# Kernel optimization log

Hardware: AMD Instinct MI355X
Metric: run time of the kernel (lower is better)

## Reference

```python
import jax, jax.numpy as jnp
import numpy as np

D = 128      # embedding dim
T = 8        # message passing rounds (config.training.T)
NV = 4000    # n_vars
NL = 2 * NV  # n_literals
NC = 16000   # n_clauses


def setup_inputs() -> dict:
    key = jax.random.key(0)
    ks = jax.random.split(key, 12)
    s = np.float32(1.0 / np.sqrt(D))
    return {
        "L_state": jax.random.normal(ks[0], (1, NL, D), jnp.float32),
        "C_state": jax.random.normal(ks[1], (1, NC, D), jnp.float32),
        "hidden_L": jnp.zeros((1, NL, D), jnp.float32),
        "hidden_C": jnp.zeros((1, NC, D), jnp.float32),
        # 0/1 literal-clause incidence, ~40 clauses per literal
        "M": (jax.random.uniform(ks[2], (NL, NC)) < 0.0025).astype(jnp.float32),
        "n_vars": NV,
        "W_lc": jax.random.normal(ks[3], (D, D), jnp.float32) * s,
        "b_lc": jnp.zeros((D,), jnp.float32),
        "W_cl": jax.random.normal(ks[4], (D, D), jnp.float32) * s,
        "b_cl": jnp.zeros((D,), jnp.float32),
        "Wih_C": jax.random.normal(ks[5], (4 * D, D), jnp.float32) * s,
        "Whh_C": jax.random.normal(ks[6], (4 * D, D), jnp.float32) * s,
        "bih_C": jnp.zeros((4 * D,), jnp.float32),
        "bhh_C": jnp.zeros((4 * D,), jnp.float32),
        "Wih_L": jax.random.normal(ks[7], (4 * D, 2 * D), jnp.float32) * s,
        "Whh_L": jax.random.normal(ks[8], (4 * D, D), jnp.float32) * s,
        "bih_L": jnp.zeros((4 * D,), jnp.float32),
        "bhh_L": jnp.zeros((4 * D,), jnp.float32),
    }


def lstm_cell(x, h, c, Wih, Whh, bih, bhh):
    # torch nn.LSTM gate order: i, f, g, o
    gates = x @ Wih.T + bih + h @ Whh.T + bhh
    i, f, g, o = jnp.split(gates, 4, axis=-1)
    c_new = jax.nn.sigmoid(f) * c + jax.nn.sigmoid(i) * jnp.tanh(g)
    h_new = jax.nn.sigmoid(o) * jnp.tanh(c_new)
    return h_new, c_new


def reference(L_state, C_state, hidden_L, hidden_C, M, n_vars,
              W_lc, b_lc, W_cl, b_cl,
              Wih_C, Whh_C, bih_C, bhh_C,
              Wih_L, Whh_L, bih_L, bhh_L):
    # Replicates torch flip() as written: slices dim 0 (size 1), so this is
    # effectively identity for n_vars >= 1 (first slice is empty, second is x).
    def flip(x):
        return jnp.concatenate([x[n_vars:2 * n_vars], x[0:n_vars]], axis=0)

    def step(carry, _):
        L, hL, hC = carry
        LC_pre = L @ W_lc.T + b_lc                        # (1, NL, D)
        LC_msgs = jnp.einsum('lc,sld->scd', M, LC_pre)    # M^T @ pre: (1, NC, D)
        Cs, hC = lstm_cell(LC_msgs, hC, hC, Wih_C, Whh_C, bih_C, bhh_C)
        CL_pre = Cs @ W_cl.T + b_cl                       # (1, NC, D)
        CL_msgs = jnp.einsum('lc,scd->sld', M, CL_pre)    # M @ pre: (1, NL, D)
        inp = jnp.concatenate([CL_msgs, flip(L)], axis=2) # (1, NL, 2D)
        L, hL = lstm_cell(inp, hL, hL, Wih_L, Whh_L, bih_L, bhh_L)
        return (L, hL, hC), None

    (L_final, _, _), _ = jax.lax.scan(step, (L_state, hidden_L, hidden_C), None, length=T)
    return L_final
```

## Files before the change

### kernel.cpp

```cpp
#include <hip/hip_runtime.h>

#define DD   128
#define NL   8000
#define NC   16000
#define TSTEPS 8
#define ROWW 96
#define COLW 64
#define OS   33
#define SPLITS8 (32 * OS)
#define SPLIT   (SPLITS8 * 8)

typedef __attribute__((ext_vector_type(8))) short short8;
typedef __attribute__((ext_vector_type(4))) float f32x4;

__device__ __forceinline__ float frcp(float x) { return __builtin_amdgcn_rcpf(x); }
__device__ __forceinline__ float sigm(float x) { return frcp(1.f + __expf(-x)); }
__device__ __forceinline__ float tanh_(float x) {
  float e = __expf(2.f * x);
  return 1.f - 2.f * frcp(e + 1.f);
}
__device__ __forceinline__ void add4(float4& a, const float4 b) {
  a.x += b.x; a.y += b.y; a.z += b.z; a.w += b.w;
}
__device__ __forceinline__ unsigned short bfround(float v) {
  unsigned u = __float_as_uint(v);
  return (unsigned short)((u + 0x7FFF + ((u >> 16) & 1)) >> 16);
}
__device__ __forceinline__ float bf2f(unsigned short b) {
  return __uint_as_float(((unsigned)b) << 16);
}
__device__ __forceinline__ int4 packi4(const unsigned short* p) {
  return make_int4(p[0] | ((int)p[1] << 16), p[2] | ((int)p[3] << 16),
                   p[4] | ((int)p[5] << 16), p[6] | ((int)p[7] << 16));
}

__device__ __forceinline__ void store_oct3(unsigned short* A, int oct, int m,
                                           float4 a, float4 b) {
  float f[8] = {a.x, a.y, a.z, a.w, b.x, b.y, b.z, b.w};
  unsigned short h[8], md[8], lo[8];
  #pragma unroll
  for (int j = 0; j < 8; ++j) {
    h[j] = bfround(f[j]);
    float r1 = f[j] - bf2f(h[j]);
    md[j] = bfround(r1);
    float r2 = r1 - bf2f(md[j]);
    lo[j] = bfround(r2);
  }
  int base = (oct * OS + m) * 8;
  *(int4*)(A + base)             = packi4(h);
  *(int4*)(A + SPLIT + base)     = packi4(md);
  *(int4*)(A + 2 * SPLIT + base) = packi4(lo);
}


__global__ __launch_bounds__(256) void copy_f4(float4* __restrict__ dst, const float4* __restrict__ src, int n4) {
  int stride = gridDim.x * blockDim.x;
  for (int i = blockIdx.x * blockDim.x + threadIdx.x; i < n4; i += stride) dst[i] = src[i];
}

__global__ __launch_bounds__(256) void scan_M(const float4* __restrict__ M4,
                                              int* __restrict__ csr, int* __restrict__ csc,
                                              int* __restrict__ rcnt, int* __restrict__ ccnt) {
  const int total = (NL * NC) / 4;
  int stride = gridDim.x * blockDim.x;
  for (int i = blockIdx.x * blockDim.x + threadIdx.x; i < total; i += stride) {
    float4 v = M4[i];
    if (v.x == 0.f && v.y == 0.f && v.z == 0.f && v.w == 0.f) continue;
    int base = i * 4;
    int l = base / NC;
    int c0 = base - l * NC;
    float vv[4] = {v.x, v.y, v.z, v.w};
    #pragma unroll
    for (int e = 0; e < 4; ++e) {
      if (vv[e] != 0.f) {
        int c = c0 + e;
        int rp = atomicAdd(&rcnt[l], 1);
        if (rp < ROWW) csr[l * ROWW + rp] = c;
        int cp = atomicAdd(&ccnt[c], 1);
        if (cp < COLW) csc[c * COLW + cp] = l;
      }
    }
  }
}

__device__ __forceinline__ void split_store(float w, int idx, unsigned short* hi,
                                            unsigned short* md, unsigned short* lo) {
  unsigned short h = bfround(w);
  float r1 = w - bf2f(h);
  unsigned short m = bfround(r1);
  float r2 = r1 - bf2f(m);
  hi[idx] = h; md[idx] = m; lo[idx] = bfround(r2);
}

__global__ __launch_bounds__(256) void build_packC(
    const float* __restrict__ WihC, const float* __restrict__ Wlc, const float* __restrict__ WhhC,
    unsigned short* __restrict__ pkhi, unsigned short* __restrict__ pkmd, unsigned short* __restrict__ pklo) {
  int i = blockIdx.x * 256 + threadIdx.x;
  int k = i >> 9, n = i & 511;
  float w;
  if (k < 128) {
    float s = 0.f;
    for (int d = 0; d < 128; ++d) s += WihC[n * 128 + d] * Wlc[d * 128 + k];
    w = s;
  } else {
    w = WhhC[n * 128 + (k - 128)];
  }
  split_store(w, ((k >> 3) * 512 + n) * 8 + (k & 7), pkhi, pkmd, pklo);
}

__global__ __launch_bounds__(256) void build_packL(
    const float* __restrict__ WihL, const float* __restrict__ Wcl, const float* __restrict__ WhhL,
    unsigned short* __restrict__ pkhi, unsigned short* __restrict__ pkmd, unsigned short* __restrict__ pklo) {
  int i = blockIdx.x * 256 + threadIdx.x;
  int k = i >> 9, n = i & 511;
  float w;
  if (k < 128) {
    float s = 0.f;
    for (int d = 0; d < 128; ++d) s += WihL[n * 256 + d] * Wcl[d * 128 + k];
    w = s;
  } else if (k < 256) {
    w = WihL[n * 256 + k];
  } else {
    w = WhhL[n * 128 + (k - 256)];
  }
  split_store(w, ((k >> 3) * 512 + n) * 8 + (k & 7), pkhi, pkmd, pklo);
}

__global__ __launch_bounds__(256) void build_bias(
    const float* __restrict__ bihC, const float* __restrict__ bhhC,
    const float* __restrict__ WihC, const float* __restrict__ blc,
    const float* __restrict__ bihL, const float* __restrict__ bhhL,
    const float* __restrict__ WihL, const float* __restrict__ bcl,
    float* __restrict__ bsumC, float* __restrict__ bvecC,
    float* __restrict__ bsumL, float* __restrict__ bvecL) {
  int i = blockIdx.x * 256 + threadIdx.x;
  if (i < 512) {
    bsumC[i] = bihC[i] + bhhC[i];
    float s = 0.f;
    for (int d = 0; d < 128; ++d) s += WihC[i * 128 + d] * blc[d];
    bvecC[i] = s;
  } else if (i < 1024) {
    int n = i - 512;
    bsumL[n] = bihL[n] + bhhL[n];
    float s = 0.f;
    for (int d = 0; d < 128; ++d) s += WihL[n * 256 + d] * bcl[d];
    bvecL[n] = s;
  }
}

#define MFMA6(ACC, AH, AM, AL, BH, BM, BL)                                   \
  ACC = __builtin_amdgcn_mfma_f32_16x16x32_bf16(AH, BH, ACC, 0, 0, 0);       \
  ACC = __builtin_amdgcn_mfma_f32_16x16x32_bf16(AH, BM, ACC, 0, 0, 0);       \
  ACC = __builtin_amdgcn_mfma_f32_16x16x32_bf16(AM, BH, ACC, 0, 0, 0);       \
  ACC = __builtin_amdgcn_mfma_f32_16x16x32_bf16(AH, BL, ACC, 0, 0, 0);       \
  ACC = __builtin_amdgcn_mfma_f32_16x16x32_bf16(AL, BH, ACC, 0, 0, 0);       \
  ACC = __builtin_amdgcn_mfma_f32_16x16x32_bf16(AM, BM, ACC, 0, 0, 0);


__global__ __launch_bounds__(512, 2) void clause_mfma(
    const float* __restrict__ Lbuf, const int* __restrict__ csc, const int* __restrict__ ccnt,
    const unsigned short* __restrict__ pkhi, const unsigned short* __restrict__ pkmd,
    const unsigned short* __restrict__ pklo,
    const float* __restrict__ bsum, const float* __restrict__ bvec,
    float* __restrict__ hC, float* __restrict__ Cs) {
  __shared__ unsigned short A[3 * SPLIT];
  const int t = threadIdx.x;
  const int rowBase = blockIdx.x * 32;

  {
    const int r = t >> 4, sub = t & 15;
    const int c = rowBase + r;
    int cnt = ccnt[c]; int cl = cnt > COLW ? COLW : cnt;
    const int* lst = csc + c * COLW;
    float4 a0 = make_float4(0, 0, 0, 0), a1 = a0;
    for (int j = 0; j < cl; ++j) {
      const float4* s4 = (const float4*)(Lbuf + (size_t)lst[j] * DD + sub * 8);
      add4(a0, s4[0]); add4(a1, s4[1]);
    }
    store_oct3(A, sub, r, a0, a1);
    const float4* h4 = (const float4*)(hC + (size_t)c * DD + sub * 8);
    store_oct3(A, 16 + sub, r, h4[0], h4[1]);
  }
  __syncthreads();

  const int w = t >> 6, l = t & 63;
  const int quad = l >> 4, lane16 = l & 15;
  const int cw = w * 16 + lane16;
  f32x4 acc[2][4];
  #pragma unroll
  for (int mt = 0; mt < 2; ++mt)
    #pragma unroll
    for (int g = 0; g < 4; ++g) acc[mt][g] = (f32x4){0.f, 0.f, 0.f, 0.f};

  const short8* As = (const short8*)A;
  const short8* Bh = (const short8*)pkhi;
  const short8* Bm = (const short8*)pkmd;
  const short8* Bl = (const short8*)pklo;

  #pragma unroll 2
  for (int s = 0; s < 8; ++s) {
    int ao = (s * 4 + quad) * OS + lane16;
    short8 a0h = As[ao],                a1h = As[ao + 16];
    short8 a0m = As[SPLITS8 + ao],      a1m = As[SPLITS8 + ao + 16];
    short8 a0l = As[2 * SPLITS8 + ao],  a1l = As[2 * SPLITS8 + ao + 16];
    int bo = (s * 4 + quad) * 512 + cw;
    #pragma unroll
    for (int g = 0; g < 4; ++g) {
      short8 bh = Bh[bo + g * 128];
      short8 bm = Bm[bo + g * 128];
      short8 bl = Bl[bo + g * 128];
      MFMA6(acc[0][g], a0h, a0m, a0l, bh, bm, bl);
      MFMA6(acc[1][g], a1h, a1m, a1l, bh, bm, bl);
    }
  }

  float bs_[4], bv_[4];
  #pragma unroll
  for (int g = 0; g < 4; ++g) { bs_[g] = bsum[g * 128 + cw]; bv_[g] = bvec[g * 128 + cw]; }
  #pragma unroll
  for (int mt = 0; mt < 2; ++mt) {
    #pragma unroll
    for (int reg = 0; reg < 4; ++reg) {
      int row = rowBase + mt * 16 + quad * 4 + reg;
      float deg = (float)ccnt[row];
      float co = hC[(size_t)row * DD + cw];
      float iv = acc[mt][0][reg] + bs_[0] + deg * bv_[0];
      float fv = acc[mt][1][reg] + bs_[1] + deg * bv_[1];
      float gv = acc[mt][2][reg] + bs_[2] + deg * bv_[2];
      float ov = acc[mt][3][reg] + bs_[3] + deg * bv_[3];
      float cn = sigm(fv) * co + sigm(iv) * tanh_(gv);
      hC[(size_t)row * DD + cw] = cn;
      Cs[(size_t)row * DD + cw] = sigm(ov) * tanh_(cn);
    }
  }
}

__global__ __launch_bounds__(512, 2) void literal_mfma(
    const float* __restrict__ Cs, const int* __restrict__ csr, const int* __restrict__ rcnt,
    const unsigned short* __restrict__ pkhi, const unsigned short* __restrict__ pkmd,
    const unsigned short* __restrict__ pklo,
    const float* __restrict__ bsum, const float* __restrict__ bvec,
    float* __restrict__ hL, float* __restrict__ Lbuf) {
  __shared__ unsigned short A[3 * SPLIT];
  const int t = threadIdx.x;
  const int rowBase = blockIdx.x * 32;
  const int r = t >> 4, sub = t & 15;
  const int lr = rowBase + r;

  {
    int cnt = rcnt[lr]; int cl = cnt > ROWW ? ROWW : cnt;
    const int* lst = csr + lr * ROWW;
    float4 a0 = make_float4(0, 0, 0, 0), a1 = a0;
    for (int j = 0; j < cl; ++j) {
      const float4* s4 = (const float4*)(Cs + (size_t)lst[j] * DD + sub * 8);
      add4(a0, s4[0]); add4(a1, s4[1]);
    }
    store_oct3(A, sub, r, a0, a1);
    const float4* l4 = (const float4*)(Lbuf + (size_t)lr * DD + sub * 8);
    store_oct3(A, 16 + sub, r, l4[0], l4[1]);
  }
  __syncthreads();

  const int w = t >> 6, l = t & 63;
  const int quad = l >> 4, lane16 = l & 15;
  const int cw = w * 16 + lane16;
  f32x4 acc[2][4];
  #pragma unroll
  for (int mt = 0; mt < 2; ++mt)
    #pragma unroll
    for (int g = 0; g < 4; ++g) acc[mt][g] = (f32x4){0.f, 0.f, 0.f, 0.f};

  const short8* As = (const short8*)A;
  const short8* Bh = (const short8*)pkhi;
  const short8* Bm = (const short8*)pkmd;
  const short8* Bl = (const short8*)pklo;

  #pragma unroll 2
  for (int s = 0; s < 8; ++s) {
    int ao = (s * 4 + quad) * OS + lane16;
    short8 a0h = As[ao],                a1h = As[ao + 16];
    short8 a0m = As[SPLITS8 + ao],      a1m = As[SPLITS8 + ao + 16];
    short8 a0l = As[2 * SPLITS8 + ao],  a1l = As[2 * SPLITS8 + ao + 16];
    int bo = (s * 4 + quad) * 512 + cw;
    #pragma unroll
    for (int g = 0; g < 4; ++g) {
      short8 bh = Bh[bo + g * 128];
      short8 bm = Bm[bo + g * 128];
      short8 bl = Bl[bo + g * 128];
      MFMA6(acc[0][g], a0h, a0m, a0l, bh, bm, bl);
      MFMA6(acc[1][g], a1h, a1m, a1l, bh, bm, bl);
    }
  }

  __syncthreads();
  {
    const float4* h4 = (const float4*)(hL + (size_t)lr * DD + sub * 8);
    store_oct3(A, sub, r, h4[0], h4[1]);
  }
  __syncthreads();

  #pragma unroll 2
  for (int s = 8; s < 12; ++s) {
    int ao = ((s - 8) * 4 + quad) * OS + lane16;
    short8 a0h = As[ao],                a1h = As[ao + 16];
    short8 a0m = As[SPLITS8 + ao],      a1m = As[SPLITS8 + ao + 16];
    short8 a0l = As[2 * SPLITS8 + ao],  a1l = As[2 * SPLITS8 + ao + 16];
    int bo = (s * 4 + quad) * 512 + cw;
    #pragma unroll
    for (int g = 0; g < 4; ++g) {
      short8 bh = Bh[bo + g * 128];
      short8 bm = Bm[bo + g * 128];
      short8 bl = Bl[bo + g * 128];
      MFMA6(acc[0][g], a0h, a0m, a0l, bh, bm, bl);
      MFMA6(acc[1][g], a1h, a1m, a1l, bh, bm, bl);
    }
  }

  float bs_[4], bv_[4];
  #pragma unroll
  for (int g = 0; g < 4; ++g) { bs_[g] = bsum[g * 128 + cw]; bv_[g] = bvec[g * 128 + cw]; }
  #pragma unroll
  for (int mt = 0; mt < 2; ++mt) {
    #pragma unroll
    for (int reg = 0; reg < 4; ++reg) {
      int row = rowBase + mt * 16 + quad * 4 + reg;
      float deg = (float)rcnt[row];
      float co = hL[(size_t)row * DD + cw];
      float iv = acc[mt][0][reg] + bs_[0] + deg * bv_[0];
      float fv = acc[mt][1][reg] + bs_[1] + deg * bv_[1];
      float gv = acc[mt][2][reg] + bs_[2] + deg * bv_[2];
      float ov = acc[mt][3][reg] + bs_[3] + deg * bv_[3];
      float cn = sigm(fv) * co + sigm(iv) * tanh_(gv);
      hL[(size_t)row * DD + cw] = cn;
      Lbuf[(size_t)row * DD + cw] = sigm(ov) * tanh_(cn);
    }
  }
}


extern "C" void kernel_launch(void* const* d_in, const int* in_sizes, int n_in,
                              void* d_out, int out_size, void* d_ws, size_t ws_size,
                              hipStream_t stream) {
  const float* L0   = (const float*)d_in[0];
  const float* hL0  = (const float*)d_in[2];
  const float* hC0  = (const float*)d_in[3];
  const float* M    = (const float*)d_in[4];
  const float* Wlc  = (const float*)d_in[6];
  const float* blc  = (const float*)d_in[7];
  const float* Wcl  = (const float*)d_in[8];
  const float* bcl  = (const float*)d_in[9];
  const float* WihC = (const float*)d_in[10];
  const float* WhhC = (const float*)d_in[11];
  const float* bihC = (const float*)d_in[12];
  const float* bhhC = (const float*)d_in[13];
  const float* WihL = (const float*)d_in[14];
  const float* WhhL = (const float*)d_in[15];
  const float* bihL = (const float*)d_in[16];
  const float* bhhL = (const float*)d_in[17];

  float* ws    = (float*)d_ws;
  float* hL    = ws;
  float* hC    = hL + NL * DD;
  float* Cs    = hC + NC * DD;
  float* bsumC = Cs + NC * DD;
  float* bvecC = bsumC + 512;
  float* bsumL = bvecC + 512;
  float* bvecL = bsumL + 512;
  unsigned short* pkChi = (unsigned short*)(bvecL + 512);
  unsigned short* pkCmd = pkChi + 256 * 512;
  unsigned short* pkClo = pkCmd + 256 * 512;
  unsigned short* pkLhi = pkClo + 256 * 512;
  unsigned short* pkLmd = pkLhi + 384 * 512;
  unsigned short* pkLlo = pkLmd + 384 * 512;
  int* csr  = (int*)(pkLlo + 384 * 512);
  int* csc  = csr + NL * ROWW;
  int* rcnt = csc + NC * COLW;
  int* ccnt = rcnt + NL;
  float* Lbuf = (float*)d_out;

  hipMemsetAsync(rcnt, 0, (NL + NC) * sizeof(int), stream);

  copy_f4<<<1024, 256, 0, stream>>>((float4*)Lbuf, (const float4*)L0,  NL * DD / 4);
  copy_f4<<<1024, 256, 0, stream>>>((float4*)hL,   (const float4*)hL0, NL * DD / 4);
  copy_f4<<<1024, 256, 0, stream>>>((float4*)hC,   (const float4*)hC0, NC * DD / 4);

  scan_M<<<4096, 256, 0, stream>>>((const float4*)M, csr, csc, rcnt, ccnt);

  build_packC<<<(256 * 512) / 256, 256, 0, stream>>>(WihC, Wlc, WhhC, pkChi, pkCmd, pkClo);
  build_packL<<<(384 * 512) / 256, 256, 0, stream>>>(WihL, Wcl, WhhL, pkLhi, pkLmd, pkLlo);
  build_bias<<<4, 256, 0, stream>>>(bihC, bhhC, WihC, blc, bihL, bhhL, WihL, bcl,
                                    bsumC, bvecC, bsumL, bvecL);

  for (int t = 0; t < TSTEPS; ++t) {
    clause_mfma<<<NC / 32, 512, 0, stream>>>(Lbuf, csc, ccnt, pkChi, pkCmd, pkClo,
                                             bsumC, bvecC, hC, Cs);
    literal_mfma<<<NL / 32, 512, 0, stream>>>(Cs, csr, rcnt, pkLhi, pkLmd, pkLlo,
                                              bsumL, bvecL, hL, Lbuf);
  }
}
```

Measured before the change: 1.473 ms.

## Fuse all message-passing steps into one persistent kernel with grid barriers

Replaces the 16 per-step clause/literal kernel launches and the three copy kernels with a single persistent kernel of 256 blocks. The blocks loop over tiles and use an atomic-counter grid barrier between phases. The literal phase now uses 16-row tiles with all three A segments held in shared memory at once, which avoids the mid-kernel reload and gives 500 tiles instead of 250. This removes launch gaps and tail effects between phases, but grid-stride tiling with 256 blocks gives uneven work per block (500 clause tiles), and the spin barrier relies on all blocks being co-resident.

```diff
diff --git a/kernel.cpp b/kernel.cpp
--- a/kernel.cpp
+++ b/kernel.cpp
@@ -6,9 +6,14 @@
 #define TSTEPS 8
 #define ROWW 96
 #define COLW 64
-#define OS   33
-#define SPLITS8 (32 * OS)
-#define SPLIT   (SPLITS8 * 8)
+#define NBLK 256
+#define CTILES (NC / 32)
+#define LTILES (NL / 16)
+
+#define CSTR 33
+#define CSPL (32 * CSTR * 8)
+#define LSTR 17
+#define LSPL (48 * LSTR * 8)
 
 typedef __attribute__((ext_vector_type(8))) short short8;
 typedef __attribute__((ext_vector_type(4))) float f32x4;
@@ -34,8 +39,8 @@
                    p[4] | ((int)p[5] << 16), p[6] | ((int)p[7] << 16));
 }
 
-__device__ __forceinline__ void store_oct3(unsigned short* A, int oct, int m,
-                                           float4 a, float4 b) {
+__device__ __forceinline__ void store_oct3C(unsigned short* A, int oct, int m,
+                                            float4 a, float4 b) {
   float f[8] = {a.x, a.y, a.z, a.w, b.x, b.y, b.z, b.w};
   unsigned short h[8], md[8], lo[8];
   #pragma unroll
@@ -46,17 +51,38 @@
     float r2 = r1 - bf2f(md[j]);
     lo[j] = bfround(r2);
   }
-  int base = (oct * OS + m) * 8;
-  *(int4*)(A + base)             = packi4(h);
-  *(int4*)(A + SPLIT + base)     = packi4(md);
-  *(int4*)(A + 2 * SPLIT + base) = packi4(lo);
-}
-
-
-__global__ __launch_bounds__(256) void copy_f4(float4* __restrict__ dst, const float4* __restrict__ src, int n4) {
-  int stride = gridDim.x * blockDim.x;
-  for (int i = blockIdx.x * blockDim.x + threadIdx.x; i < n4; i += stride) dst[i] = src[i];
-}
+  int base = (oct * CSTR + m) * 8;
+  *(int4*)(A + base)            = packi4(h);
+  *(int4*)(A + CSPL + base)     = packi4(md);
+  *(int4*)(A + 2 * CSPL + base) = packi4(lo);
+}
+
+__device__ __forceinline__ void store_half3L(unsigned short* A, int oct, int half, int m,
+                                             float4 a) {
+  float f[4] = {a.x, a.y, a.z, a.w};
+  unsigned short h[4], md[4], lo[4];
+  #pragma unroll
+  for (int j = 0; j < 4; ++j) {
+    h[j] = bfround(f[j]);
+    float r1 = f[j] - bf2f(h[j]);
+    md[j] = bfround(r1);
+    float r2 = r1 - bf2f(md[j]);
+    lo[j] = bfround(r2);
+  }
+  int base = (oct * LSTR + m) * 8 + half * 4;
+  *(int2*)(A + base)            = make_int2(h[0]  | ((int)h[1]  << 16), h[2]  | ((int)h[3]  << 16));
+  *(int2*)(A + LSPL + base)     = make_int2(md[0] | ((int)md[1] << 16), md[2] | ((int)md[3] << 16));
+  *(int2*)(A + 2 * LSPL + base) = make_int2(lo[0] | ((int)lo[1] << 16), lo[2] | ((int)lo[3] << 16));
+}
+
+#define MFMA6(ACC, AH, AM, AL, BH, BM, BL)                                   \
+  ACC = __builtin_amdgcn_mfma_f32_16x16x32_bf16(AH, BH, ACC, 0, 0, 0);       \
+  ACC = __builtin_amdgcn_mfma_f32_16x16x32_bf16(AH, BM, ACC, 0, 0, 0);       \
+  ACC = __builtin_amdgcn_mfma_f32_16x16x32_bf16(AM, BH, ACC, 0, 0, 0);       \
+  ACC = __builtin_amdgcn_mfma_f32_16x16x32_bf16(AH, BL, ACC, 0, 0, 0);       \
+  ACC = __builtin_amdgcn_mfma_f32_16x16x32_bf16(AL, BH, ACC, 0, 0, 0);       \
+  ACC = __builtin_amdgcn_mfma_f32_16x16x32_bf16(AM, BM, ACC, 0, 0, 0);
+
 
 __global__ __launch_bounds__(256) void scan_M(const float4* __restrict__ M4,
                                               int* __restrict__ csr, int* __restrict__ csc,
@@ -148,191 +174,181 @@
   }
 }
 
-#define MFMA6(ACC, AH, AM, AL, BH, BM, BL)                                   \
-  ACC = __builtin_amdgcn_mfma_f32_16x16x32_bf16(AH, BH, ACC, 0, 0, 0);       \
-  ACC = __builtin_amdgcn_mfma_f32_16x16x32_bf16(AH, BM, ACC, 0, 0, 0);       \
-  ACC = __builtin_amdgcn_mfma_f32_16x16x32_bf16(AM, BH, ACC, 0, 0, 0);       \
-  ACC = __builtin_amdgcn_mfma_f32_16x16x32_bf16(AH, BL, ACC, 0, 0, 0);       \
-  ACC = __builtin_amdgcn_mfma_f32_16x16x32_bf16(AL, BH, ACC, 0, 0, 0);       \
-  ACC = __builtin_amdgcn_mfma_f32_16x16x32_bf16(AM, BM, ACC, 0, 0, 0);
-
-
-__global__ __launch_bounds__(512, 2) void clause_mfma(
-    const float* __restrict__ Lbuf, const int* __restrict__ csc, const int* __restrict__ ccnt,
-    const unsigned short* __restrict__ pkhi, const unsigned short* __restrict__ pkmd,
-    const unsigned short* __restrict__ pklo,
-    const float* __restrict__ bsum, const float* __restrict__ bvec,
-    float* __restrict__ hC, float* __restrict__ Cs) {
-  __shared__ unsigned short A[3 * SPLIT];
+__device__ __forceinline__ void grid_barrier(int* cnt, int& gen) {
+  __syncthreads();
+  if (threadIdx.x == 0) {
+    __threadfence();
+    ++gen;
+    __hip_atomic_fetch_add(cnt, 1, __ATOMIC_ACQ_REL, __HIP_MEMORY_SCOPE_AGENT);
+    while (__hip_atomic_load(cnt, __ATOMIC_ACQUIRE, __HIP_MEMORY_SCOPE_AGENT) < gen * NBLK)
+      __builtin_amdgcn_s_sleep(1);
+    __threadfence();
+  }
+  __syncthreads();
+}
+
+
+__global__ __launch_bounds__(512, 4) void fused_steps(
+    const float* __restrict__ L0, const float* __restrict__ hL0, const float* __restrict__ hC0,
+    const int* __restrict__ csr, const int* __restrict__ csc,
+    const int* __restrict__ rcnt, const int* __restrict__ ccnt,
+    const unsigned short* __restrict__ pkChi, const unsigned short* __restrict__ pkCmd,
+    const unsigned short* __restrict__ pkClo,
+    const unsigned short* __restrict__ pkLhi, const unsigned short* __restrict__ pkLmd,
+    const unsigned short* __restrict__ pkLlo,
+    const float* __restrict__ bsumC, const float* __restrict__ bvecC,
+    const float* __restrict__ bsumL, const float* __restrict__ bvecL,
+    float* __restrict__ hL, float* __restrict__ hC, float* __restrict__ Cs,
+    float* __restrict__ Lbuf, int* __restrict__ bar) {
+  __shared__ unsigned short A[3 * CSPL];
+
   const int t = threadIdx.x;
-  const int rowBase = blockIdx.x * 32;
-
-  {
-    const int r = t >> 4, sub = t & 15;
-    const int c = rowBase + r;
-    int cnt = ccnt[c]; int cl = cnt > COLW ? COLW : cnt;
-    const int* lst = csc + c * COLW;
-    float4 a0 = make_float4(0, 0, 0, 0), a1 = a0;
-    for (int j = 0; j < cl; ++j) {
-      const float4* s4 = (const float4*)(Lbuf + (size_t)lst[j] * DD + sub * 8);
-      add4(a0, s4[0]); add4(a1, s4[1]);
-    }
-    store_oct3(A, sub, r, a0, a1);
-    const float4* h4 = (const float4*)(hC + (size_t)c * DD + sub * 8);
-    store_oct3(A, 16 + sub, r, h4[0], h4[1]);
-  }
-  __syncthreads();
-
+  const int b = blockIdx.x;
   const int w = t >> 6, l = t & 63;
   const int quad = l >> 4, lane16 = l & 15;
   const int cw = w * 16 + lane16;
-  f32x4 acc[2][4];
-  #pragma unroll
-  for (int mt = 0; mt < 2; ++mt)
-    #pragma unroll
-    for (int g = 0; g < 4; ++g) acc[mt][g] = (f32x4){0.f, 0.f, 0.f, 0.f};
-
-  const short8* As = (const short8*)A;
-  const short8* Bh = (const short8*)pkhi;
-  const short8* Bm = (const short8*)pkmd;
-  const short8* Bl = (const short8*)pklo;
-
-  #pragma unroll 2
-  for (int s = 0; s < 8; ++s) {
-    int ao = (s * 4 + quad) * OS + lane16;
-    short8 a0h = As[ao],                a1h = As[ao + 16];
-    short8 a0m = As[SPLITS8 + ao],      a1m = As[SPLITS8 + ao + 16];
-    short8 a0l = As[2 * SPLITS8 + ao],  a1l = As[2 * SPLITS8 + ao + 16];
-    int bo = (s * 4 + quad) * 512 + cw;
-    #pragma unroll
-    for (int g = 0; g < 4; ++g) {
-      short8 bh = Bh[bo + g * 128];
-      short8 bm = Bm[bo + g * 128];
-      short8 bl = Bl[bo + g * 128];
-      MFMA6(acc[0][g], a0h, a0m, a0l, bh, bm, bl);
-      MFMA6(acc[1][g], a1h, a1m, a1l, bh, bm, bl);
+  int gen = 0;
+
+  {
+    int gid = b * 512 + t, gstr = NBLK * 512;
+    for (int i = gid; i < NL * DD / 4; i += gstr) ((float4*)Lbuf)[i] = ((const float4*)L0)[i];
+    for (int i = gid; i < NL * DD / 4; i += gstr) ((float4*)hL)[i]   = ((const float4*)hL0)[i];
+    for (int i = gid; i < NC * DD / 4; i += gstr) ((float4*)hC)[i]   = ((const float4*)hC0)[i];
+  }
+
+  for (int step = 0; step < TSTEPS; ++step) {
+    grid_barrier(bar, gen);
+
+    for (int tile = b; tile < CTILES; tile += NBLK) {
+      const int rowBase = tile * 32;
+      {
+        const int r = t >> 4, sub = t & 15;
+        const int c = rowBase + r;
+        int cnt = ccnt[c]; int cl2 = cnt > COLW ? COLW : cnt;
+        const int* lst = csc + c * COLW;
+        float4 a0 = make_float4(0, 0, 0, 0), a1 = a0;
+        for (int j = 0; j < cl2; ++j) {
+          const float4* s4 = (const float4*)(Lbuf + (size_t)lst[j] * DD + sub * 8);
+          add4(a0, s4[0]); add4(a1, s4[1]);
+        }
+        store_oct3C(A, sub, r, a0, a1);
+        const float4* h4 = (const float4*)(hC + (size_t)c * DD + sub * 8);
+        store_oct3C(A, 16 + sub, r, h4[0], h4[1]);
+      }
+      __syncthreads();
+
+      f32x4 acc[2][4];
+      #pragma unroll
+      for (int mt = 0; mt < 2; ++mt)
+        #pragma unroll
+        for (int g = 0; g < 4; ++g) acc[mt][g] = (f32x4){0.f, 0.f, 0.f, 0.f};
+
+      const short8* As = (const short8*)A;
+      const short8* Bh = (const short8*)pkChi;
+      const short8* Bm = (const short8*)pkCmd;
+      const short8* Bl = (const short8*)pkClo;
+
+      #pragma unroll 2
+      for (int s = 0; s < 8; ++s) {
+        int ao = (s * 4 + quad) * CSTR + lane16;
+        short8 a0h = As[ao],                   a1h = As[ao + 16];
+        short8 a0m = As[CSPL / 8 + ao],        a1m = As[CSPL / 8 + ao + 16];
+        short8 a0l = As[2 * (CSPL / 8) + ao],  a1l = As[2 * (CSPL / 8) + ao + 16];
+        int bo = (s * 4 + quad) * 512 + cw;
+        #pragma unroll
+        for (int g = 0; g < 4; ++g) {
+          short8 bh = Bh[bo + g * 128];
+          short8 bm = Bm[bo + g * 128];
+          short8 bl = Bl[bo + g * 128];
+          MFMA6(acc[0][g], a0h, a0m, a0l, bh, bm, bl);
+          MFMA6(acc[1][g], a1h, a1m, a1l, bh, bm, bl);
+        }
+      }
+
+      float bs_[4], bv_[4];
+      #pragma unroll
+      for (int g = 0; g < 4; ++g) { bs_[g] = bsumC[g * 128 + cw]; bv_[g] = bvecC[g * 128 + cw]; }
+      #pragma unroll
+      for (int mt = 0; mt < 2; ++mt) {
+        #pragma unroll
+        for (int reg = 0; reg < 4; ++reg) {
+          int row = rowBase + mt * 16 + quad * 4 + reg;
+          float deg = (float)ccnt[row];
+          float co = hC[(size_t)row * DD + cw];
+          float iv = acc[mt][0][reg] + bs_[0] + deg * bv_[0];
+          float fv = acc[mt][1][reg] + bs_[1] + deg * bv_[1];
+          float gv = acc[mt][2][reg] + bs_[2] + deg * bv_[2];
+          float ov = acc[mt][3][reg] + bs_[3] + deg * bv_[3];
+          float cn = sigm(fv) * co + sigm(iv) * tanh_(gv);
+          hC[(size_t)row * DD + cw] = cn;
+          Cs[(size_t)row * DD + cw] = sigm(ov) * tanh_(cn);
+        }
+      }
+      __syncthreads();
     }
-  }
-
-  float bs_[4], bv_[4];
-  #pragma unroll
-  for (int g = 0; g < 4; ++g) { bs_[g] = bsum[g * 128 + cw]; bv_[g] = bvec[g * 128 + cw]; }
-  #pragma unroll
-  for (int mt = 0; mt < 2; ++mt) {
-    #pragma unroll
-    for (int reg = 0; reg < 4; ++reg) {
-      int row = rowBase + mt * 16 + quad * 4 + reg;
-      float deg = (float)ccnt[row];
-      float co = hC[(size_t)row * DD + cw];
-      float iv = acc[mt][0][reg] + bs_[0] + deg * bv_[0];
-      float fv = acc[mt][1][reg] + bs_[1] + deg * bv_[1];
-      float gv = acc[mt][2][reg] + bs_[2] + deg * bv_[2];
-      float ov = acc[mt][3][reg] + bs_[3] + deg * bv_[3];
-      float cn = sigm(fv) * co + sigm(iv) * tanh_(gv);
-      hC[(size_t)row * DD + cw] = cn;
-      Cs[(size_t)row * DD + cw] = sigm(ov) * tanh_(cn);
-    }
-  }
-}
-
-__global__ __launch_bounds__(512, 2) void literal_mfma(
-    const float* __restrict__ Cs, const int* __restrict__ csr, const int* __restrict__ rcnt,
-    const unsigned short* __restrict__ pkhi, const unsigned short* __restrict__ pkmd,
-    const unsigned short* __restrict__ pklo,
-    const float* __restrict__ bsum, const float* __restrict__ bvec,
-    float* __restrict__ hL, float* __restrict__ Lbuf) {
-  __shared__ unsigned short A[3 * SPLIT];
-  const int t = threadIdx.x;
-  const int rowBase = blockIdx.x * 32;
-  const int r = t >> 4, sub = t & 15;
-  const int lr = rowBase + r;
-
-  {
-    int cnt = rcnt[lr]; int cl = cnt > ROWW ? ROWW : cnt;
-    const int* lst = csr + lr * ROWW;
-    float4 a0 = make_float4(0, 0, 0, 0), a1 = a0;
-    for (int j = 0; j < cl; ++j) {
-      const float4* s4 = (const float4*)(Cs + (size_t)lst[j] * DD + sub * 8);
-      add4(a0, s4[0]); add4(a1, s4[1]);
-    }
-    store_oct3(A, sub, r, a0, a1);
-    const float4* l4 = (const float4*)(Lbuf + (size_t)lr * DD + sub * 8);
-    store_oct3(A, 16 + sub, r, l4[0], l4[1]);
-  }
-  __syncthreads();
-
-  const int w = t >> 6, l = t & 63;
-  const int quad = l >> 4, lane16 = l & 15;
-  const int cw = w * 16 + lane16;
-  f32x4 acc[2][4];
-  #pragma unroll
-  for (int mt = 0; mt < 2; ++mt)
-    #pragma unroll
-    for (int g = 0; g < 4; ++g) acc[mt][g] = (f32x4){0.f, 0.f, 0.f, 0.f};
-
-  const short8* As = (const short8*)A;
-  const short8* Bh = (const short8*)pkhi;
-  const short8* Bm = (const short8*)pkmd;
-  const short8* Bl = (const short8*)pklo;
-
-  #pragma unroll 2
-  for (int s = 0; s < 8; ++s) {
-    int ao = (s * 4 + quad) * OS + lane16;
-    short8 a0h = As[ao],                a1h = As[ao + 16];
-    short8 a0m = As[SPLITS8 + ao],      a1m = As[SPLITS8 + ao + 16];
-    short8 a0l = As[2 * SPLITS8 + ao],  a1l = As[2 * SPLITS8 + ao + 16];
-    int bo = (s * 4 + quad) * 512 + cw;
-    #pragma unroll
-    for (int g = 0; g < 4; ++g) {
-      short8 bh = Bh[bo + g * 128];
-      short8 bm = Bm[bo + g * 128];
-      short8 bl = Bl[bo + g * 128];
-      MFMA6(acc[0][g], a0h, a0m, a0l, bh, bm, bl);
-      MFMA6(acc[1][g], a1h, a1m, a1l, bh, bm, bl);
-    }
-  }
-
-  __syncthreads();
-  {
-    const float4* h4 = (const float4*)(hL + (size_t)lr * DD + sub * 8);
-    store_oct3(A, sub, r, h4[0], h4[1]);
-  }
-  __syncthreads();
-
-  #pragma unroll 2
-  for (int s = 8; s < 12; ++s) {
-    int ao = ((s - 8) * 4 + quad) * OS + lane16;
-    short8 a0h = As[ao],                a1h = As[ao + 16];
-    short8 a0m = As[SPLITS8 + ao],      a1m = As[SPLITS8 + ao + 16];
-    short8 a0l = As[2 * SPLITS8 + ao],  a1l = As[2 * SPLITS8 + ao + 16];
-    int bo = (s * 4 + quad) * 512 + cw;
-    #pragma unroll
-    for (int g = 0; g < 4; ++g) {
-      short8 bh = Bh[bo + g * 128];
-      short8 bm = Bm[bo + g * 128];
-      short8 bl = Bl[bo + g * 128];
-      MFMA6(acc[0][g], a0h, a0m, a0l, bh, bm, bl);
-      MFMA6(acc[1][g], a1h, a1m, a1l, bh, bm, bl);
-    }
-  }
-
-  float bs_[4], bv_[4];
-  #pragma unroll
-  for (int g = 0; g < 4; ++g) { bs_[g] = bsum[g * 128 + cw]; bv_[g] = bvec[g * 128 + cw]; }
-  #pragma unroll
-  for (int mt = 0; mt < 2; ++mt) {
-    #pragma unroll
-    for (int reg = 0; reg < 4; ++reg) {
-      int row = rowBase + mt * 16 + quad * 4 + reg;
-      float deg = (float)rcnt[row];
-      float co = hL[(size_t)row * DD + cw];
-      float iv = acc[mt][0][reg] + bs_[0] + deg * bv_[0];
-      float fv = acc[mt][1][reg] + bs_[1] + deg * bv_[1];
-      float gv = acc[mt][2][reg] + bs_[2] + deg * bv_[2];
-      float ov = acc[mt][3][reg] + bs_[3] + deg * bv_[3];
-      float cn = sigm(fv) * co + sigm(iv) * tanh_(gv);
-      hL[(size_t)row * DD + cw] = cn;
-      Lbuf[(size_t)row * DD + cw] = sigm(ov) * tanh_(cn);
+
+    grid_barrier(bar, gen);
+
+    for (int tile = b; tile < LTILES; tile += NBLK) {
+      const int rowBase = tile * 16;
+      {
+        const int r = t >> 5, cg2 = t & 31;
+        const int lr = rowBase + r;
+        int cnt = rcnt[lr]; int cl2 = cnt > ROWW ? ROWW : cnt;
+        const int* lst = csr + lr * ROWW;
+        float4 a0 = make_float4(0, 0, 0, 0);
+        for (int j = 0; j < cl2; ++j)
+          add4(a0, ((const float4*)(Cs + (size_t)lst[j] * DD))[cg2]);
+        store_half3L(A, cg2 >> 1, cg2 & 1, r, a0);
+        store_half3L(A, 16 + (cg2 >> 1), cg2 & 1, r,
+                     ((const float4*)(Lbuf + (size_t)lr * DD))[cg2]);
+        store_half3L(A, 32 + (cg2 >> 1), cg2 & 1, r,
+                     ((const float4*)(hL + (size_t)lr * DD))[cg2]);
+      }
+      __syncthreads();
+
+      f32x4 acc[4];
+      #pragma unroll
+      for (int g = 0; g < 4; ++g) acc[g] = (f32x4){0.f, 0.f, 0.f, 0.f};
+
+      const short8* As = (const short8*)A;
+      const short8* Bh = (const short8*)pkLhi;
+      const short8* Bm = (const short8*)pkLmd;
+      const short8* Bl = (const short8*)pkLlo;
+
+      #pragma unroll 2
+      for (int s = 0; s < 12; ++s) {
+        int ao = (s * 4 + quad) * LSTR + lane16;
+        short8 ah = As[ao];
+        short8 am = As[LSPL / 8 + ao];
+        short8 al = As[2 * (LSPL / 8) + ao];
+        int bo = (s * 4 + quad) * 512 + cw;
+        #pragma unroll
+        for (int g = 0; g < 4; ++g) {
+          short8 bh = Bh[bo + g * 128];
+          short8 bm = Bm[bo + g * 128];
+          short8 bl = Bl[bo + g * 128];
+          MFMA6(acc[g], ah, am, al, bh, bm, bl);
+        }
+      }
+
+      float bs_[4], bv_[4];
+      #pragma unroll
+      for (int g = 0; g < 4; ++g) { bs_[g] = bsumL[g * 128 + cw]; bv_[g] = bvecL[g * 128 + cw]; }
+      #pragma unroll
+      for (int reg = 0; reg < 4; ++reg) {
+        int row = rowBase + quad * 4 + reg;
+        float deg = (float)rcnt[row];
+        float co = hL[(size_t)row * DD + cw];
+        float iv = acc[0][reg] + bs_[0] + deg * bv_[0];
+        float fv = acc[1][reg] + bs_[1] + deg * bv_[1];
+        float gv = acc[2][reg] + bs_[2] + deg * bv_[2];
+        float ov = acc[3][reg] + bs_[3] + deg * bv_[3];
+        float cn = sigm(fv) * co + sigm(iv) * tanh_(gv);
+        hL[(size_t)row * DD + cw] = cn;
+        Lbuf[(size_t)row * DD + cw] = sigm(ov) * tanh_(cn);
+      }
+      __syncthreads();
     }
   }
 }
@@ -376,25 +392,20 @@
   int* csc  = csr + NL * ROWW;
   int* rcnt = csc + NC * COLW;
   int* ccnt = rcnt + NL;
+  int* bar  = ccnt + NC;
   float* Lbuf = (float*)d_out;
 
-  hipMemsetAsync(rcnt, 0, (NL + NC) * sizeof(int), stream);
-
-  copy_f4<<<1024, 256, 0, stream>>>((float4*)Lbuf, (const float4*)L0,  NL * DD / 4);
-  copy_f4<<<1024, 256, 0, stream>>>((float4*)hL,   (const float4*)hL0, NL * DD / 4);
-  copy_f4<<<1024, 256, 0, stream>>>((float4*)hC,   (const float4*)hC0, NC * DD / 4);
+  hipMemsetAsync(rcnt, 0, (NL + NC + 1) * sizeof(int), stream);
 
   scan_M<<<4096, 256, 0, stream>>>((const float4*)M, csr, csc, rcnt, ccnt);
-
   build_packC<<<(256 * 512) / 256, 256, 0, stream>>>(WihC, Wlc, WhhC, pkChi, pkCmd, pkClo);
   build_packL<<<(384 * 512) / 256, 256, 0, stream>>>(WihL, Wcl, WhhL, pkLhi, pkLmd, pkLlo);
   build_bias<<<4, 256, 0, stream>>>(bihC, bhhC, WihC, blc, bihL, bhhL, WihL, bcl,
                                     bsumC, bvecC, bsumL, bvecL);
 
-  for (int t = 0; t < TSTEPS; ++t) {
-    clause_mfma<<<NC / 32, 512, 0, stream>>>(Lbuf, csc, ccnt, pkChi, pkCmd, pkClo,
-                                             bsumC, bvecC, hC, Cs);
-    literal_mfma<<<NL / 32, 512, 0, stream>>>(Cs, csr, rcnt, pkLhi, pkLmd, pkLlo,
-                                              bsumL, bvecL, hL, Lbuf);
-  }
-}
+  fused_steps<<<NBLK, 512, 0, stream>>>(
+      L0, hL0, hC0, csr, csc, rcnt, ccnt,
+      pkChi, pkCmd, pkClo, pkLhi, pkLmd, pkLlo,
+      bsumC, bvecC, bsumL, bvecL,
+      hL, hC, Cs, Lbuf, bar);
+}
```

New measurement: 2.552 ms. 73.2% more time.

## Halve literal tile rows, stage index lists in LDS, batch gather loads

Applied to the files above, without the earlier changes.

The literal kernel now handles 16 rows per block, giving twice as many blocks, and stages the full 384-wide K dimension (messages, L, hL) in LDS at once. That removes the second LDS pass and its extra barriers, so one MFMA loop covers all 12 K-steps. Both kernels copy their CSR/CSC index lists into shared memory and unroll the gather eight-wide so several loads are in flight at once, and the clause MFMA loop is fully unrolled. The cost is higher register pressure and twice as many reads of the weight tiles in the literal kernel, since each block now covers fewer rows.

```diff
diff --git a/kernel.cpp b/kernel.cpp
--- a/kernel.cpp
+++ b/kernel.cpp
@@ -6,9 +6,12 @@
 #define TSTEPS 8
 #define ROWW 96
 #define COLW 64
+
 #define OS   33
 #define SPLITS8 (32 * OS)
 #define SPLIT   (SPLITS8 * 8)
+#define LSTR 17
+#define LSPL (48 * LSTR * 8)
 
 typedef __attribute__((ext_vector_type(8))) short short8;
 typedef __attribute__((ext_vector_type(4))) float f32x4;
@@ -51,6 +54,32 @@
   *(int4*)(A + SPLIT + base)     = packi4(md);
   *(int4*)(A + 2 * SPLIT + base) = packi4(lo);
 }
+
+__device__ __forceinline__ void store_half3L(unsigned short* A, int oct, int half, int m,
+                                             float4 a) {
+  float f[4] = {a.x, a.y, a.z, a.w};
+  unsigned short h[4], md[4], lo[4];
+  #pragma unroll
+  for (int j = 0; j < 4; ++j) {
+    h[j] = bfround(f[j]);
+    float r1 = f[j] - bf2f(h[j]);
+    md[j] = bfround(r1);
+    float r2 = r1 - bf2f(md[j]);
+    lo[j] = bfround(r2);
+  }
+  int base = (oct * LSTR + m) * 8 + half * 4;
+  *(int2*)(A + base)            = make_int2(h[0]  | ((int)h[1]  << 16), h[2]  | ((int)h[3]  << 16));
+  *(int2*)(A + LSPL + base)     = make_int2(md[0] | ((int)md[1] << 16), md[2] | ((int)md[3] << 16));
+  *(int2*)(A + 2 * LSPL + base) = make_int2(lo[0] | ((int)lo[1] << 16), lo[2] | ((int)lo[3] << 16));
+}
+
+#define MFMA6(ACC, AH, AM, AL, BH, BM, BL)                                   \
+  ACC = __builtin_amdgcn_mfma_f32_16x16x32_bf16(AH, BH, ACC, 0, 0, 0);       \
+  ACC = __builtin_amdgcn_mfma_f32_16x16x32_bf16(AH, BM, ACC, 0, 0, 0);       \
+  ACC = __builtin_amdgcn_mfma_f32_16x16x32_bf16(AM, BH, ACC, 0, 0, 0);       \
+  ACC = __builtin_amdgcn_mfma_f32_16x16x32_bf16(AH, BL, ACC, 0, 0, 0);       \
+  ACC = __builtin_amdgcn_mfma_f32_16x16x32_bf16(AL, BH, ACC, 0, 0, 0);       \
+  ACC = __builtin_amdgcn_mfma_f32_16x16x32_bf16(AM, BM, ACC, 0, 0, 0);
 
 
 __global__ __launch_bounds__(256) void copy_f4(float4* __restrict__ dst, const float4* __restrict__ src, int n4) {
@@ -148,14 +177,6 @@
   }
 }
 
-#define MFMA6(ACC, AH, AM, AL, BH, BM, BL)                                   \
-  ACC = __builtin_amdgcn_mfma_f32_16x16x32_bf16(AH, BH, ACC, 0, 0, 0);       \
-  ACC = __builtin_amdgcn_mfma_f32_16x16x32_bf16(AH, BM, ACC, 0, 0, 0);       \
-  ACC = __builtin_amdgcn_mfma_f32_16x16x32_bf16(AM, BH, ACC, 0, 0, 0);       \
-  ACC = __builtin_amdgcn_mfma_f32_16x16x32_bf16(AH, BL, ACC, 0, 0, 0);       \
-  ACC = __builtin_amdgcn_mfma_f32_16x16x32_bf16(AL, BH, ACC, 0, 0, 0);       \
-  ACC = __builtin_amdgcn_mfma_f32_16x16x32_bf16(AM, BM, ACC, 0, 0, 0);
-
 
 __global__ __launch_bounds__(512, 2) void clause_mfma(
     const float* __restrict__ Lbuf, const int* __restrict__ csc, const int* __restrict__ ccnt,
@@ -164,21 +185,36 @@
     const float* __restrict__ bsum, const float* __restrict__ bvec,
     float* __restrict__ hC, float* __restrict__ Cs) {
   __shared__ unsigned short A[3 * SPLIT];
+  __shared__ int IDX[32 * COLW];
   const int t = threadIdx.x;
   const int rowBase = blockIdx.x * 32;
+
+  ((int4*)IDX)[t] = ((const int4*)(csc + rowBase * COLW))[t];
+  __syncthreads();
 
   {
     const int r = t >> 4, sub = t & 15;
     const int c = rowBase + r;
-    int cnt = ccnt[c]; int cl = cnt > COLW ? COLW : cnt;
-    const int* lst = csc + c * COLW;
+    int cnt = ccnt[c]; if (cnt > COLW) cnt = COLW;
+    const int* lst = IDX + r * COLW;
     float4 a0 = make_float4(0, 0, 0, 0), a1 = a0;
-    for (int j = 0; j < cl; ++j) {
-      const float4* s4 = (const float4*)(Lbuf + (size_t)lst[j] * DD + sub * 8);
+    int j = 0;
+    for (; j + 8 <= cnt; j += 8) {
+      float4 p0[8], p1[8];
+      #pragma unroll
+      for (int u = 0; u < 8; ++u) {
+        const float4* s4 = (const float4*)(Lbuf + (size_t)lst[j + u] * DD) + sub * 2;
+        p0[u] = s4[0]; p1[u] = s4[1];
+      }
+      #pragma unroll
+      for (int u = 0; u < 8; ++u) { add4(a0, p0[u]); add4(a1, p1[u]); }
+    }
+    for (; j < cnt; ++j) {
+      const float4* s4 = (const float4*)(Lbuf + (size_t)lst[j] * DD) + sub * 2;
       add4(a0, s4[0]); add4(a1, s4[1]);
     }
     store_oct3(A, sub, r, a0, a1);
-    const float4* h4 = (const float4*)(hC + (size_t)c * DD + sub * 8);
+    const float4* h4 = (const float4*)(hC + (size_t)c * DD) + sub * 2;
     store_oct3(A, 16 + sub, r, h4[0], h4[1]);
   }
   __syncthreads();
@@ -197,7 +233,7 @@
   const short8* Bm = (const short8*)pkmd;
   const short8* Bl = (const short8*)pklo;
 
-  #pragma unroll 2
+  #pragma unroll
   for (int s = 0; s < 8; ++s) {
     int ao = (s * 4 + quad) * OS + lane16;
     short8 a0h = As[ao],                a1h = As[ao + 16];
@@ -241,78 +277,64 @@
     const unsigned short* __restrict__ pklo,
     const float* __restrict__ bsum, const float* __restrict__ bvec,
     float* __restrict__ hL, float* __restrict__ Lbuf) {
-  __shared__ unsigned short A[3 * SPLIT];
+  __shared__ unsigned short A[3 * LSPL];
+  __shared__ int IDX[16 * ROWW];
   const int t = threadIdx.x;
-  const int rowBase = blockIdx.x * 32;
-  const int r = t >> 4, sub = t & 15;
-  const int lr = rowBase + r;
+  const int rowBase = blockIdx.x * 16;
+
+  if (t < 384) ((int4*)IDX)[t] = ((const int4*)(csr + rowBase * ROWW))[t];
+  __syncthreads();
 
   {
-    int cnt = rcnt[lr]; int cl = cnt > ROWW ? ROWW : cnt;
-    const int* lst = csr + lr * ROWW;
-    float4 a0 = make_float4(0, 0, 0, 0), a1 = a0;
-    for (int j = 0; j < cl; ++j) {
-      const float4* s4 = (const float4*)(Cs + (size_t)lst[j] * DD + sub * 8);
-      add4(a0, s4[0]); add4(a1, s4[1]);
-    }
-    store_oct3(A, sub, r, a0, a1);
-    const float4* l4 = (const float4*)(Lbuf + (size_t)lr * DD + sub * 8);
-    store_oct3(A, 16 + sub, r, l4[0], l4[1]);
+    const int r = t >> 5, cg2 = t & 31;
+    const int lr = rowBase + r;
+    int cnt = rcnt[lr]; if (cnt > ROWW) cnt = ROWW;
+    const int* lst = IDX + r * ROWW;
+    float4 a0 = make_float4(0, 0, 0, 0);
+    int j = 0;
+    for (; j + 8 <= cnt; j += 8) {
+      float4 p[8];
+      #pragma unroll
+      for (int u = 0; u < 8; ++u)
+        p[u] = ((const float4*)(Cs + (size_t)lst[j + u] * DD))[cg2];
+      #pragma unroll
+      for (int u = 0; u < 8; ++u) add4(a0, p[u]);
+    }
+    for (; j < cnt; ++j)
+      add4(a0, ((const float4*)(Cs + (size_t)lst[j] * DD))[cg2]);
+    store_half3L(A, cg2 >> 1, cg2 & 1, r, a0);
+    store_half3L(A, 16 + (cg2 >> 1), cg2 & 1, r,
+                 ((const float4*)(Lbuf + (size_t)lr * DD))[cg2]);
+    store_half3L(A, 32 + (cg2 >> 1), cg2 & 1, r,
+                 ((const float4*)(hL + (size_t)lr * DD))[cg2]);
   }
   __syncthreads();
 
   const int w = t >> 6, l = t & 63;
   const int quad = l >> 4, lane16 = l & 15;
   const int cw = w * 16 + lane16;
-  f32x4 acc[2][4];
-  #pragma unroll
-  for (int mt = 0; mt < 2; ++mt)
-    #pragma unroll
-    for (int g = 0; g < 4; ++g) acc[mt][g] = (f32x4){0.f, 0.f, 0.f, 0.f};
+  f32x4 acc[4];
+  #pragma unroll
+  for (int g = 0; g < 4; ++g) acc[g] = (f32x4){0.f, 0.f, 0.f, 0.f};
 
   const short8* As = (const short8*)A;
   const short8* Bh = (const short8*)pkhi;
   const short8* Bm = (const short8*)pkmd;
   const short8* Bl = (const short8*)pklo;
 
-  #pragma unroll 2
-  for (int s = 0; s < 8; ++s) {
-    int ao = (s * 4 + quad) * OS + lane16;
-    short8 a0h = As[ao],                a1h = As[ao + 16];
-    short8 a0m = As[SPLITS8 + ao],      a1m = As[SPLITS8 + ao + 16];
-    short8 a0l = As[2 * SPLITS8 + ao],  a1l = As[2 * SPLITS8 + ao + 16];
+  #pragma unroll
+  for (int s = 0; s < 12; ++s) {
+    int ao = (s * 4 + quad) * LSTR + lane16;
+    short8 ah = As[ao];
+    short8 am = As[LSPL / 8 + ao];
+    short8 al = As[2 * (LSPL / 8) + ao];
     int bo = (s * 4 + quad) * 512 + cw;
     #pragma unroll
     for (int g = 0; g < 4; ++g) {
       short8 bh = Bh[bo + g * 128];
       short8 bm = Bm[bo + g * 128];
       short8 bl = Bl[bo + g * 128];
-      MFMA6(acc[0][g], a0h, a0m, a0l, bh, bm, bl);
-      MFMA6(acc[1][g], a1h, a1m, a1l, bh, bm, bl);
-    }
-  }
-
-  __syncthreads();
-  {
-    const float4* h4 = (const float4*)(hL + (size_t)lr * DD + sub * 8);
-    store_oct3(A, sub, r, h4[0], h4[1]);
-  }
-  __syncthreads();
-
-  #pragma unroll 2
-  for (int s = 8; s < 12; ++s) {
-    int ao = ((s - 8) * 4 + quad) * OS + lane16;
-    short8 a0h = As[ao],                a1h = As[ao + 16];
-    short8 a0m = As[SPLITS8 + ao],      a1m = As[SPLITS8 + ao + 16];
-    short8 a0l = As[2 * SPLITS8 + ao],  a1l = As[2 * SPLITS8 + ao + 16];
-    int bo = (s * 4 + quad) * 512 + cw;
-    #pragma unroll
-    for (int g = 0; g < 4; ++g) {
-      short8 bh = Bh[bo + g * 128];
-      short8 bm = Bm[bo + g * 128];
-      short8 bl = Bl[bo + g * 128];
-      MFMA6(acc[0][g], a0h, a0m, a0l, bh, bm, bl);
-      MFMA6(acc[1][g], a1h, a1m, a1l, bh, bm, bl);
+      MFMA6(acc[g], ah, am, al, bh, bm, bl);
     }
   }
 
@@ -320,20 +342,17 @@
   #pragma unroll
   for (int g = 0; g < 4; ++g) { bs_[g] = bsum[g * 128 + cw]; bv_[g] = bvec[g * 128 + cw]; }
   #pragma unroll
-  for (int mt = 0; mt < 2; ++mt) {
-    #pragma unroll
-    for (int reg = 0; reg < 4; ++reg) {
-      int row = rowBase + mt * 16 + quad * 4 + reg;
-      float deg = (float)rcnt[row];
-      float co = hL[(size_t)row * DD + cw];
-      float iv = acc[mt][0][reg] + bs_[0] + deg * bv_[0];
-      float fv = acc[mt][1][reg] + bs_[1] + deg * bv_[1];
-      float gv = acc[mt][2][reg] + bs_[2] + deg * bv_[2];
-      float ov = acc[mt][3][reg] + bs_[3] + deg * bv_[3];
-      float cn = sigm(fv) * co + sigm(iv) * tanh_(gv);
-      hL[(size_t)row * DD + cw] = cn;
-      Lbuf[(size_t)row * DD + cw] = sigm(ov) * tanh_(cn);
-    }
+  for (int reg = 0; reg < 4; ++reg) {
+    int row = rowBase + quad * 4 + reg;
+    float deg = (float)rcnt[row];
+    float co = hL[(size_t)row * DD + cw];
+    float iv = acc[0][reg] + bs_[0] + deg * bv_[0];
+    float fv = acc[1][reg] + bs_[1] + deg * bv_[1];
+    float gv = acc[2][reg] + bs_[2] + deg * bv_[2];
+    float ov = acc[3][reg] + bs_[3] + deg * bv_[3];
+    float cn = sigm(fv) * co + sigm(iv) * tanh_(gv);
+    hL[(size_t)row * DD + cw] = cn;
+    Lbuf[(size_t)row * DD + cw] = sigm(ov) * tanh_(cn);
   }
 }
 
@@ -394,7 +413,7 @@
   for (int t = 0; t < TSTEPS; ++t) {
     clause_mfma<<<NC / 32, 512, 0, stream>>>(Lbuf, csc, ccnt, pkChi, pkCmd, pkClo,
                                              bsumC, bvecC, hC, Cs);
-    literal_mfma<<<NL / 32, 512, 0, stream>>>(Cs, csr, rcnt, pkLhi, pkLmd, pkLlo,
+    literal_mfma<<<NL / 16, 512, 0, stream>>>(Cs, csr, rcnt, pkLhi, pkLmd, pkLlo,
                                               bsumL, bvecL, hL, Lbuf);
   }
 }
```

Result: faster. 1.359 ms (-7.8%).
